# Performance work log

Measured on AMD Instinct MI355X. Metric: run time of the kernel, lower is better.

The kernel has to match this reference:

```python
import jax, jax.numpy as jnp
import numpy as np

B, LD = 256, 64
NO, LO = 10240, 32
NM, LM = 81920, 16
EO, EM = 81920, 327680
E, HID, H, Dh, V = 128, 256, 8, 16, 10000


def masked_mean(tokens, table):
    # tokens: [N, L] int; pad id = 0
    emb = table[tokens]                            # [N, L, E]
    mask = (tokens != 0)
    s = jnp.sum(emb * mask[..., None].astype(emb.dtype), axis=1)
    lens = jnp.maximum(jnp.sum(mask, axis=1), 1).astype(emb.dtype)
    return s / lens[:, None]


def segment_softmax(scores, seg, num_segments):
    # scores: [E, ...]; softmax over entries sharing seg id (PyG softmax)
    m = jax.ops.segment_max(scores, seg, num_segments=num_segments)
    e = jnp.exp(scores - m[seg])
    s = jax.ops.segment_sum(e, seg, num_segments=num_segments)
    return e / (s[seg] + 1e-16)


def gcn_conv(x, W, b, src, dst, n):
    # PyG GCNConv: normalize=True, add_self_loops=True
    xw = x @ W
    loops = jnp.arange(n, dtype=src.dtype)
    s2 = jnp.concatenate([src, loops])
    d2 = jnp.concatenate([dst, loops])
    deg = jax.ops.segment_sum(jnp.ones_like(d2, dtype=x.dtype), d2, num_segments=n)
    dinv = deg ** -0.5  # deg >= 1 due to self loops
    norm = dinv[s2] * dinv[d2]
    out = jax.ops.segment_sum(xw[s2] * norm[:, None], d2, num_segments=n)
    return out + b


def transformer_conv(x, Wq, bq, Wk, bk, Wv, bv, Wskip, bskip, src, dst, n):
    q = (x @ Wq + bq).reshape(n, H, Dh)
    k = (x @ Wk + bk).reshape(n, H, Dh)
    v = (x @ Wv + bv).reshape(n, H, Dh)
    score = jnp.sum(q[dst] * k[src], axis=-1) / jnp.sqrt(jnp.asarray(Dh, x.dtype))  # [E, H]
    alpha = segment_softmax(score, dst, n)
    agg = jax.ops.segment_sum(alpha[:, :, None] * v[src], dst, num_segments=n)  # [n, H, Dh]
    return agg.reshape(n, H * Dh) + x @ Wskip + bskip


def global_attention(x, Wg, bg, seg, num_segments):
    gate = x @ Wg + bg                              # [N, 1]
    a = segment_softmax(gate, seg, num_segments)
    return jax.ops.segment_sum(a * x, seg, num_segments=num_segments)


def setup_inputs():
    key = jax.random.key(0)
    ks = jax.random.split(key, 20)
    sc = lambda k, shape: jax.random.normal(k, shape, dtype=jnp.float32) * 0.05
    inp = {
        "desc_tokens": jax.random.randint(ks[0], (B, LD), 0, V, dtype=jnp.int32),
        "x_tokens": jax.random.randint(ks[1], (NO, LO), 0, V, dtype=jnp.int32),
        "mini_tokens": jax.random.randint(ks[2], (NM, LM), 0, V, dtype=jnp.int32),
        "src": jax.random.randint(ks[3], (EO,), 0, NO, dtype=jnp.int32),
        "dst": jax.random.randint(ks[4], (EO,), 0, NO, dtype=jnp.int32),
        "mini_src": jax.random.randint(ks[5], (EM,), 0, NM, dtype=jnp.int32),
        "mini_dst": jax.random.randint(ks[6], (EM,), 0, NM, dtype=jnp.int32),
        "mini_batch": (jnp.arange(NM, dtype=jnp.int32) // (NM // NO)),
        "node_batch": (jnp.arange(NO, dtype=jnp.int32) // (NO // B)),
        "desc_table": sc(ks[7], (V, E)),
        "code_table": sc(ks[8], (V, E)),
        "code_table2": sc(ks[9], (V, E)),
        "Wq": sc(ks[10], (E, H * Dh)), "bq": jnp.zeros((H * Dh,), jnp.float32),
        "Wk": sc(ks[11], (E, H * Dh)), "bk": jnp.zeros((H * Dh,), jnp.float32),
        "Wv": sc(ks[12], (E, H * Dh)), "bv": jnp.zeros((H * Dh,), jnp.float32),
        "Wskip": sc(ks[13], (E, H * Dh)), "bskip": jnp.zeros((H * Dh,), jnp.float32),
        "W2": sc(ks[14], (E, HID)), "b2": jnp.zeros((HID,), jnp.float32),
        "W3": sc(ks[15], (HID, E)), "b3": jnp.zeros((E,), jnp.float32),
        "Wg": sc(ks[16], (E, 1)), "bg": jnp.zeros((1,), jnp.float32),
    }
    return inp


def reference(desc_tokens, x_tokens, mini_tokens, src, dst, mini_src, mini_dst,
              mini_batch, node_batch, desc_table, code_table, code_table2,
              Wq, bq, Wk, bk, Wv, bv, Wskip, bskip, W2, b2, W3, b3, Wg, bg):
    # encode_desc: embedding + masked mean pool -> [B, E]
    h_n = masked_mean(desc_tokens, desc_table)
    # encode_code_graph
    stmt_emb = masked_mean(x_tokens, code_table2)          # [NO, E]
    mini_emb = masked_mean(mini_tokens, code_table)        # [NM, E]
    mini_hidden = transformer_conv(mini_emb, Wq, bq, Wk, bk, Wv, bv,
                                   Wskip, bskip, mini_src, mini_dst, NM)
    mini_fn = global_attention(mini_hidden, Wg, bg, mini_batch, NO)  # [NO, E]
    mini_fn = (mini_fn + stmt_emb) * 0.5
    h = jax.nn.relu(gcn_conv(mini_fn, W2, b2, src, dst, NO))
    final_stmt = gcn_conv(h, W3, b3, src, dst, NO)
    fn_repr = global_attention(final_stmt, Wg, bg, node_batch, B)    # [B, E]
    # cosine similarity (torch eps=1e-8 clamps each norm)
    na = jnp.maximum(jnp.linalg.norm(fn_repr, axis=-1), 1e-8)
    nb = jnp.maximum(jnp.linalg.norm(h_n, axis=-1), 1e-8)
    return jnp.sum(fn_repr * h_n, axis=-1) / (na * nb)
```

## Files before the change

### kernel.cpp

```cpp
#include <hip/hip_runtime.h>
#include <hip/hip_bf16.h>
#include <math.h>

#define BB   256
#define LDE  64
#define NO   10240
#define LO   32
#define NM   81920
#define LM   16
#define EO   81920
#define EM   327680
#define ED   128
#define HIDD 256
#define NH   8
#define DH   16
#define VV   10000

static inline int nblk(long long n, int b) { return (int)((n + b - 1) / b); }

typedef __attribute__((ext_vector_type(8))) short short8;
typedef __attribute__((ext_vector_type(4))) float f32x4;

static __device__ __forceinline__ unsigned short bf16_rne(float f) {
  unsigned u = __float_as_uint(f);
  return (unsigned short)((u + 0x7fffu + ((u >> 16) & 1u)) >> 16);
}
static __device__ __forceinline__ float bf16_to_f(unsigned short h) {
  return __uint_as_float(((unsigned)h) << 16);
}
static __device__ __forceinline__ float4 b4f(ushort4 h) {
  return make_float4(bf16_to_f(h.x), bf16_to_f(h.y), bf16_to_f(h.z), bf16_to_f(h.w));
}
static __device__ __forceinline__ ushort4 f4b(float4 v) {
  return make_ushort4(bf16_rne(v.x), bf16_rne(v.y), bf16_rne(v.z), bf16_rne(v.w));
}

static __device__ __forceinline__ void gl_lds16(const void* g, void* l) {
  __builtin_amdgcn_global_load_lds(
      (const __attribute__((address_space(1))) unsigned int*)g,
      (__attribute__((address_space(3))) unsigned int*)l, 16, 0, 0);
}

struct ConvArgs {
  const float *Wq, *Wk, *Wv, *Ws, *W2, *W3;
  const float *bq, *bk, *bv, *bs;
  short8* frag;
  float* bias512;
  const float* t1; unsigned short* o1;
  const float* t2; unsigned short* o2;
  int* hist;
};
#define TBLK (2 * VV * ED / 4 / 256)
#define ZBLK ((NM + NO) / 256)
__global__ void __launch_bounds__(256)
conv_all_k(ConvArgs A) {
  int b = blockIdx.x;
  if (b < 32) {
    int g = b * 256 + threadIdx.x;
    int lane = g & 63, f = g >> 6;
    int jl = f & 7, kb = (f >> 3) & 3, ch = f >> 5;
    int cf = ch * 8 + jl;
    int c = cf * 16 + (lane & 15);
    int k0 = kb * 32 + ((lane >> 4) << 3);
    const float* wp; int cm;
    if (c < 128)      { wp = A.Wq; cm = c; }
    else if (c < 384) { int u = c - 128, t = u & 7;
                        wp = (t < 4) ? A.Wk : A.Wv; cm = (u >> 3) * 4 + (t & 3); }
    else              { wp = A.Ws; cm = c - 384; }
    short8 h;
    #pragma unroll
    for (int j = 0; j < 8; ++j)
      h[j] = (short)bf16_rne(wp[(size_t)(k0 + j) * 128 + cm]);
    A.frag[g] = h;
  } else if (b < 64) {
    int g = (b - 32) * 256 + threadIdx.x;
    const float* wp; int M, dstbase, gg;
    if (g < 4096) { wp = A.W2; M = 256; dstbase = 8192;  gg = g; }
    else          { wp = A.W3; M = 128; dstbase = 12288; gg = g - 4096; }
    int lane = gg & 63, fid = gg >> 6;
    int nt = fid % (M / 16), kb = fid / (M / 16);
    int n = nt * 16 + (lane & 15);
    int k0 = kb * 32 + ((lane >> 4) << 3);
    short8 h;
    #pragma unroll
    for (int j = 0; j < 8; ++j)
      h[j] = (short)bf16_rne(wp[(size_t)(k0 + j) * M + n]);
    A.frag[dstbase + gg] = h;
  } else if (b < 64 + TBLK) {
    int q = (b - 64) * 256 + threadIdx.x;
    const int NT = VV * ED / 4;
    if (q < NT) {
      float4 v = *(const float4*)(A.t1 + (size_t)q * 4);
      *(ushort4*)(A.o1 + (size_t)q * 4) = f4b(v);
    } else if (q < 2 * NT) {
      int q2 = q - NT;
      float4 v = *(const float4*)(A.t2 + (size_t)q2 * 4);
      *(ushort4*)(A.o2 + (size_t)q2 * 4) = f4b(v);
    }
  } else if (b < 64 + TBLK + ZBLK) {
    int i = (b - 64 - TBLK) * 256 + threadIdx.x;
    if (i < NM + NO) A.hist[i] = 0;
  } else {
    for (int c = threadIdx.x; c < 512; c += 256) {
      float v;
      if (c < 128)      v = A.bq[c];
      else if (c < 384) { int u = c - 128, t = u & 7;
                          v = (t < 4) ? A.bk[(u >> 3) * 4 + t] : A.bv[(u >> 3) * 4 + (t & 3)]; }
      else              v = A.bs[c - 384];
      A.bias512[c] = v;
    }
  }
}

template<int L>
static __device__ __forceinline__ void embed_body_f(const int* __restrict__ tokens,
                                                    const float* __restrict__ table,
                                                    float* __restrict__ out, int blk) {
  const int r = threadIdx.x >> 5, lane = threadIdx.x & 31;
  const int n0 = blk * 8;
  __shared__ int toks[8][L];
  for (int i = threadIdx.x; i < 8 * L; i += 256)
    toks[i / L][i % L] = tokens[(size_t)n0 * L + i];
  __syncthreads();
  float4 acc = make_float4(0.f, 0.f, 0.f, 0.f);
  int cnt = 0;
  #pragma unroll
  for (int l = 0; l < L; ++l) {
    int t = toks[r][l];
    float4 v = *(const float4*)(table + (size_t)t * ED + lane * 4);
    float msk = (t != 0) ? 1.f : 0.f;
    cnt += (t != 0);
    acc.x = fmaf(msk, v.x, acc.x); acc.y = fmaf(msk, v.y, acc.y);
    acc.z = fmaf(msk, v.z, acc.z); acc.w = fmaf(msk, v.w, acc.w);
  }
  float inv = 1.f / (float)(cnt > 0 ? cnt : 1);
  acc.x *= inv; acc.y *= inv; acc.z *= inv; acc.w *= inv;
  *(float4*)(out + (size_t)(n0 + r) * ED + lane * 4) = acc;
}

template<int L>
static __device__ __forceinline__ void embed_body16(const int* __restrict__ tokens,
                                                    const unsigned short* __restrict__ table,
                                                    unsigned short* __restrict__ out, int blk) {
  const int r = threadIdx.x >> 4, lane = threadIdx.x & 15;
  const int n0 = blk * 16;
  __shared__ int toks[16][L];
  for (int i = threadIdx.x; i < 16 * L; i += 256)
    toks[i / L][i % L] = tokens[(size_t)n0 * L + i];
  __syncthreads();
  float acc[8] = {};
  int cnt = 0;
  #pragma unroll
  for (int l = 0; l < L; ++l) {
    int t = toks[r][l];
    short8 v = *(const short8*)(table + (size_t)t * ED + lane * 8);
    float msk = (t != 0) ? 1.f : 0.f;
    cnt += (t != 0);
    #pragma unroll
    for (int j = 0; j < 8; ++j)
      acc[j] = fmaf(msk, bf16_to_f((unsigned short)v[j]), acc[j]);
  }
  float inv = 1.f / (float)(cnt > 0 ? cnt : 1);
  short8 o;
  #pragma unroll
  for (int j = 0; j < 8; ++j) o[j] = (short)bf16_rne(acc[j] * inv);
  *(short8*)(out + (size_t)(n0 + r) * ED + lane * 8) = o;
}

#define HBLK ((EM + EO) / 256)
__global__ void __launch_bounds__(256)
embed_all_k(const int* __restrict__ desc_tokens, const float* __restrict__ desc_table,
            float* __restrict__ h_n,
            const int* __restrict__ x_tokens, const unsigned short* __restrict__ ctab2,
            unsigned short* __restrict__ stmt,
            const int* __restrict__ mini_tokens, const unsigned short* __restrict__ ctab,
            unsigned short* __restrict__ miniE,
            const int* __restrict__ mini_dst, const int* __restrict__ dst,
            int* __restrict__ histm, int* __restrict__ histo) {
  int b = blockIdx.x;
  if (b < HBLK) {
    int e = b * 256 + threadIdx.x;
    if (e < EM) atomicAdd(&histm[mini_dst[e]], 1);
    else        atomicAdd(&histo[dst[e - EM]], 1);
  }
  else if (b < HBLK + BB / 8) embed_body_f<LDE>(desc_tokens, desc_table, h_n, b - HBLK);
  else if (b < HBLK + BB / 8 + NO / 16)
    embed_body16<LO>(x_tokens, ctab2, stmt, b - HBLK - BB / 8);
  else embed_body16<LM>(mini_tokens, ctab, miniE, b - HBLK - BB / 8 - NO / 16);
}

__global__ void chunk_sum_k(const int* __restrict__ hist, int* __restrict__ partials, int N) {
  __shared__ int sd[256];
  int i = blockIdx.x * 256 + threadIdx.x;
  sd[threadIdx.x] = (i < N) ? hist[i] : 0;
  __syncthreads();
  for (int s = 128; s > 0; s >>= 1) {
    if (threadIdx.x < s) sd[threadIdx.x] += sd[threadIdx.x + s];
    __syncthreads();
  }
  if (threadIdx.x == 0) partials[blockIdx.x] = sd[0];
}
__global__ void scan_partials2_k(int* __restrict__ p) {
  __shared__ int sd[512];
  int base = (blockIdx.x == 0) ? 0 : NM / 256;
  int B    = (blockIdx.x == 0) ? NM / 256 : NO / 256;
  int t = threadIdx.x;
  int v = (t < B) ? p[base + t] : 0;
  sd[t] = v; __syncthreads();
  for (int off = 1; off < 512; off <<= 1) {
    int a = (t >= off) ? sd[t - off] : 0;
    __syncthreads();
    sd[t] += a;
    __syncthreads();
  }
  if (t < B) p[base + t] = sd[t] - v;
}
__global__ void scan_final2_k(const int* __restrict__ hist, const int* __restrict__ partials,
                              int* __restrict__ offsm, int* __restrict__ curm,
                              int* __restrict__ offso, int* __restrict__ curo,
                              float* __restrict__ dinv) {
  __shared__ int sd[256];
  int i = blockIdx.x * 256 + threadIdx.x;
  int v = hist[i];
  sd[threadIdx.x] = v; __syncthreads();
  for (int off = 1; off < 256; off <<= 1) {
    int a = (threadIdx.x >= off) ? sd[threadIdx.x - off] : 0;
    __syncthreads();
    sd[threadIdx.x] += a;
    __syncthreads();
  }
  int excl = sd[threadIdx.x] - v + partials[blockIdx.x];
  if (i < NM) {
    offsm[i] = excl; curm[i] = excl;
    if (i == NM - 1) offsm[NM] = excl + v;
  } else {
    int i2 = i - NM;
    offso[i2] = excl; curo[i2] = excl;
    if (i2 == NO - 1) offso[NO] = excl + v;
    dinv[i2] = 1.f / sqrtf(1.f + (float)v);
  }
}
__global__ void scatter2_k(const int* __restrict__ sm, const int* __restrict__ dm,
                           int* __restrict__ cm, int* __restrict__ km,
                           const int* __restrict__ so, const int* __restrict__ dd,
                           int* __restrict__ co, int* __restrict__ ko) {
  int e = blockIdx.x * 256 + threadIdx.x;
  if (e < EM) {
    int pos = atomicAdd(&cm[dm[e]], 1);
    km[pos] = sm[e];
  } else {
    int e2 = e - EM;
    if (e2 < EO) {
      int pos = atomicAdd(&co[dd[e2]], 1);
      ko[pos] = so[e2];
    }
  }
}

__global__ void __launch_bounds__(512)
qkvs_merged_k(const unsigned short* __restrict__ Ab, const short8* __restrict__ Wf,
              const float* __restrict__ bias512, unsigned short* __restrict__ out) {
  const int id = blockIdx.x;
  const int blk = (id & 7) * 80 + (id >> 3);
  const int n0 = blk * 128;
  const int tid = threadIdx.x;
  const int w = tid >> 6, lane = tid & 63;
  const int r = lane & 15, qd = lane >> 4;
  const int node = n0 + w * 16 + r;
  __shared__ short8 wlds[2048];
  char* myl = (char*)wlds + w * 4096;

  short8 a[4];
  #pragma unroll
  for (int kb = 0; kb < 4; ++kb)
    a[kb] = *(const short8*)(Ab + (size_t)node * ED + kb * 32 + qd * 8);

  for (int ch = 0; ch < 4; ++ch) {
    {
      const char* gs = (const char*)Wf + (size_t)ch * 32768
                     + (size_t)(w * 4) * 1024 + (size_t)lane * 16;
      char* ls = (char*)wlds + (w * 4) * 1024;
      #pragma unroll
      for (int t = 0; t < 4; ++t)
        gl_lds16(gs + t * 1024, ls + t * 1024);
    }
    __syncthreads();

    f32x4 acc[8];
    #pragma unroll
    for (int jl = 0; jl < 8; ++jl) acc[jl] = (f32x4){0.f, 0.f, 0.f, 0.f};
    #pragma unroll
    for (int kb = 0; kb < 4; ++kb)
      #pragma unroll
      for (int jl = 0; jl < 8; ++jl) {
        short8 wf = *(const short8*)((const char*)wlds
                      + ((size_t)((kb << 3) | jl) * 64 + lane) * 16);
        acc[jl] = __builtin_amdgcn_mfma_f32_16x16x32_bf16(wf, a[kb], acc[jl], 0, 0, 0);
      }
    __syncthreads();

    #pragma unroll
    for (int jl = 0; jl < 8; ++jl) {
      const int cf = ch * 8 + jl;
      const float4 bv = *(const float4*)(bias512 + cf * 16 + qd * 4);
      ushort4 o;
      o.x = bf16_rne(acc[jl][0] + bv.x);
      o.y = bf16_rne(acc[jl][1] + bv.y);
      o.z = bf16_rne(acc[jl][2] + bv.z);
      o.w = bf16_rne(acc[jl][3] + bv.w);
      *(ushort4*)(myl + r * 256 + ((jl * 32) ^ ((r & 7) << 5)) + qd * 8) = o;
    }
    #pragma unroll
    for (int t = 0; t < 4; ++t) {
      const int rr = t * 4 + qd;
      short8 v = *(const short8*)(myl + rr * 256 + (((lane & 15) * 16) ^ ((rr & 7) << 5)));
      *(short8*)(out + (size_t)(n0 + w * 16 + rr) * 512 + ch * 128 + (lane & 15) * 8) = v;
    }
    __syncthreads();
  }
}

template<bool RELU>
__global__ void __launch_bounds__(512)
mgemm_b_k(const unsigned short* __restrict__ Ab, const short8* __restrict__ Bh,
          const float* __restrict__ bias, unsigned short* __restrict__ C,
          int K, int M) {
  const int bn0 = blockIdx.x * 128;
  const int n0 = blockIdx.y * 128;
  const int tid = threadIdx.x;
  const int w = tid >> 6, lane = tid & 63;
  const int wm = (w & 3) * 2, wn = (w >> 2) * 4;
  const int r = lane & 15, qd = lane >> 4;
  const int NTm = M / 16;
  f32x4 acc[2][4];
  #pragma unroll
  for (int i = 0; i < 2; ++i)
    #pragma unroll
    for (int j = 0; j < 4; ++j) acc[i][j] = (f32x4){0.f, 0.f, 0.f, 0.f};
  const int kbn = K / 32;
  for (int kb = 0; kb < kbn; ++kb) {
    short8 bh[4];
    #pragma unroll
    for (int j = 0; j < 4; ++j)
      bh[j] = Bh[((size_t)kb * NTm + (bn0 >> 4) + wn + j) * 64 + lane];
    short8 a[2];
    #pragma unroll
    for (int i = 0; i < 2; ++i)
      a[i] = *(const short8*)(Ab + (size_t)(n0 + (wm + i) * 16 + r) * K + kb * 32 + qd * 8);
    #pragma unroll
    for (int i = 0; i < 2; ++i)
      #pragma unroll
      for (int j = 0; j < 4; ++j)
        acc[i][j] = __builtin_amdgcn_mfma_f32_16x16x32_bf16(bh[j], a[i], acc[i][j], 0, 0, 0);
  }
  #pragma unroll
  for (int i = 0; i < 2; ++i)
    #pragma unroll
    for (int j = 0; j < 4; ++j) {
      const int node = n0 + (wm + i) * 16 + r;
      const int colb = bn0 + (wn + j) * 16 + qd * 4;
      float4 bv = bias ? *(const float4*)(bias + colb) : make_float4(0.f, 0.f, 0.f, 0.f);
      float v0 = acc[i][j][0] + bv.x;
      float v1 = acc[i][j][1] + bv.y;
      float v2 = acc[i][j][2] + bv.z;
      float v3 = acc[i][j][3] + bv.w;
      if (RELU) {
        v0 = fmaxf(v0, 0.f); v1 = fmaxf(v1, 0.f);
        v2 = fmaxf(v2, 0.f); v3 = fmaxf(v3, 0.f);
      }
      ushort4 o = make_ushort4(bf16_rne(v0), bf16_rne(v1), bf16_rne(v2), bf16_rne(v3));
      *(ushort4*)(C + (size_t)node * M + colb) = o;
    }
}

__global__ void __launch_bounds__(128)
attn_fused_k(unsigned short* buf,
             const int* __restrict__ offs, const int* __restrict__ csr,
             const float* __restrict__ Wg, const float* __restrict__ bg,
             float* __restrict__ gateOut) {
  const int g = threadIdx.x >> 5, lane = threadIdx.x & 31;
  const int n = blockIdx.x * 4 + g;
  float4 q = b4f(*(const ushort4*)(buf + (size_t)n * 512 + lane * 4));
  float4 sk = b4f(*(const ushort4*)(buf + (size_t)n * 512 + 384 + lane * 4));
  float4 wg = *(const float4*)(Wg + lane * 4);
  int lo = offs[n], hi = offs[n + 1];
  float4 O = make_float4(0.f, 0.f, 0.f, 0.f);
  float m = -INFINITY, l = 0.f;
  for (int base = lo; base < hi; base += 4) {
    int rem = hi - base;
    int sidx[4];
    #pragma unroll
    for (int i = 0; i < 4; ++i) sidx[i] = (i < rem) ? csr[base + i] : 0;
    short8 kvr[4];
    #pragma unroll
    for (int i = 0; i < 4; ++i)
      kvr[i] = *(const short8*)(buf + (size_t)sidx[i] * 512 + 128 + lane * 8);
    float sc[4]; float4 vt[4];
    #pragma unroll
    for (int i = 0; i < 4; ++i) {
      float4 kt = make_float4(bf16_to_f((unsigned short)kvr[i][0]),
                              bf16_to_f((unsigned short)kvr[i][1]),
                              bf16_to_f((unsigned short)kvr[i][2]),
                              bf16_to_f((unsigned short)kvr[i][3]));
      vt[i] = make_float4(bf16_to_f((unsigned short)kvr[i][4]),
                          bf16_to_f((unsigned short)kvr[i][5]),
                          bf16_to_f((unsigned short)kvr[i][6]),
                          bf16_to_f((unsigned short)kvr[i][7]));
      float p = q.x * kt.x + q.y * kt.y + q.z * kt.z + q.w * kt.w;
      p += __shfl_xor(p, 1, 64);
      p += __shfl_xor(p, 2, 64);
      sc[i] = (i < rem) ? p * 0.25f : -INFINITY;
    }
    float mt = fmaxf(fmaxf(sc[0], sc[1]), fmaxf(sc[2], sc[3]));
    float mn = fmaxf(m, mt);
    float scale = __expf(m - mn);
    float pe[4];
    #pragma unroll
    for (int i = 0; i < 4; ++i) pe[i] = __expf(sc[i] - mn);
    l = l * scale + ((pe[0] + pe[1]) + (pe[2] + pe[3]));
    O.x = fmaf(pe[3], vt[3].x, fmaf(pe[2], vt[2].x, fmaf(pe[1], vt[1].x, fmaf(pe[0], vt[0].x, O.x * scale))));
    O.y = fmaf(pe[3], vt[3].y, fmaf(pe[2], vt[2].y, fmaf(pe[1], vt[1].y, fmaf(pe[0], vt[0].y, O.y * scale))));
    O.z = fmaf(pe[3], vt[3].z, fmaf(pe[2], vt[2].z, fmaf(pe[1], vt[1].z, fmaf(pe[0], vt[0].z, O.z * scale))));
    O.w = fmaf(pe[3], vt[3].w, fmaf(pe[2], vt[2].w, fmaf(pe[1], vt[1].w, fmaf(pe[0], vt[0].w, O.w * scale))));
    m = mn;
  }
  float inv = 1.f / (l + 1e-16f);
  float4 out = make_float4(O.x * inv + sk.x, O.y * inv + sk.y,
                           O.z * inv + sk.z, O.w * inv + sk.w);
  *(ushort4*)(buf + (size_t)n * 512 + lane * 4) = f4b(out);
  float ps = out.x * wg.x + out.y * wg.y + out.z * wg.z + out.w * wg.w;
  #pragma unroll
  for (int o = 1; o <= 16; o <<= 1) ps += __shfl_xor(ps, o, 64);
  if (lane == 0) gateOut[n] = ps + bg[0];
}

__global__ void __launch_bounds__(256)
gcn_gather_b_k(const unsigned short* __restrict__ x, const float* __restrict__ dinv,
               const int* __restrict__ offs, const int* __restrict__ csr,
               const float* __restrict__ bias, unsigned short* __restrict__ out,
               const float* __restrict__ Wg, const float* __restrict__ bg,
               float* __restrict__ gateOut) {
  const int wv = threadIdx.x >> 6, lane = threadIdx.x & 63;
  const int half = lane >> 5, cl = lane & 31;
  const int n = blockIdx.x * 4 + wv;
  float di = dinv[n];
  float4 acc = make_float4(0.f, 0.f, 0.f, 0.f);
  if (half == 0) {
    float4 xs = b4f(*(const ushort4*)(x + (size_t)n * ED + cl * 4));
    float w0 = di * di;
    acc = make_float4(w0 * xs.x, w0 * xs.y, w0 * xs.z, w0 * xs.w);
  }
  int lo = offs[n], hi = offs[n + 1];
  for (int base = lo; base < hi; base += 8) {
    int sidx[4]; bool ok[4];
    #pragma unroll
    for (int i = 0; i < 4; ++i) {
      int e = base + 2 * i + half;
      ok[i] = e < hi;
      sidx[i] = ok[i] ? csr[e] : 0;
    }
    float dw[4];
    #pragma unroll
    for (int i = 0; i < 4; ++i) dw[i] = ok[i] ? di * dinv[sidx[i]] : 0.f;
    ushort4 vr[4];
    #pragma unroll
    for (int i = 0; i < 4; ++i)
      vr[i] = *(const ushort4*)(x + (size_t)sidx[i] * ED + cl * 4);
    #pragma unroll
    for (int i = 0; i < 4; ++i) {
      float4 v = b4f(vr[i]);
      acc.x = fmaf(dw[i], v.x, acc.x); acc.y = fmaf(dw[i], v.y, acc.y);
      acc.z = fmaf(dw[i], v.z, acc.z); acc.w = fmaf(dw[i], v.w, acc.w);
    }
  }
  acc.x += __shfl_xor(acc.x, 32, 64); acc.y += __shfl_xor(acc.y, 32, 64);
  acc.z += __shfl_xor(acc.z, 32, 64); acc.w += __shfl_xor(acc.w, 32, 64);
  if (bias) {
    float4 b4 = *(const float4*)(bias + cl * 4);
    acc.x += b4.x; acc.y += b4.y; acc.z += b4.z; acc.w += b4.w;
  }
  if (half == 0)
    *(ushort4*)(out + (size_t)n * ED + cl * 4) = f4b(acc);
  if (gateOut) {
    float4 wg = *(const float4*)(Wg + cl * 4);
    float ps = acc.x * wg.x + acc.y * wg.y + acc.z * wg.z + acc.w * wg.w;
    #pragma unroll
    for (int o = 1; o <= 16; o <<= 1) ps += __shfl_xor(ps, o, 64);
    if (lane == 0) gateOut[n] = ps + bg[0];
  }
}

static __device__ __forceinline__ int lower_bound_d(const int* a, int n, int key) {
  int lo = 0, hi = n;
  while (lo < hi) { int mid = (lo + hi) >> 1; if (a[mid] < key) lo = mid + 1; else hi = mid; }
  return lo;
}
__global__ void __launch_bounds__(128)
gattn_comb_b_k(const unsigned short* __restrict__ xv, const float* __restrict__ gate,
               const int* __restrict__ seg, int Ntot,
               const unsigned short* __restrict__ other, unsigned short* __restrict__ out) {
  const int g = threadIdx.x >> 5, lane = threadIdx.x & 31;
  const int n = blockIdx.x * 4 + g;
  __shared__ int sh[4][2];
  if (lane == 0) {
    sh[g][0] = lower_bound_d(seg, Ntot, n);
    sh[g][1] = lower_bound_d(seg, Ntot, n + 1);
  }
  __syncthreads();
  int lo = sh[g][0], hi = sh[g][1];
  float m = -INFINITY;
  for (int j = lo; j < hi; ++j) m = fmaxf(m, gate[j]);
  float ssum = 0.f;
  for (int j = lo; j < hi; ++j) ssum += __expf(gate[j] - m);
  float inv = 1.f / (ssum + 1e-16f);
  float4 acc = make_float4(0.f, 0.f, 0.f, 0.f);
  for (int j = lo; j < hi; ++j) {
    float a = __expf(gate[j] - m) * inv;
    float4 v = b4f(*(const ushort4*)(xv + (size_t)j * 512 + lane * 4));
    acc.x = fmaf(a, v.x, acc.x); acc.y = fmaf(a, v.y, acc.y);
    acc.z = fmaf(a, v.z, acc.z); acc.w = fmaf(a, v.w, acc.w);
  }
  float4 o4 = b4f(*(const ushort4*)(other + (size_t)n * ED + lane * 4));
  acc.x = (acc.x + o4.x) * 0.5f; acc.y = (acc.y + o4.y) * 0.5f;
  acc.z = (acc.z + o4.z) * 0.5f; acc.w = (acc.w + o4.w) * 0.5f;
  *(ushort4*)(out + (size_t)n * ED + lane * 4) = f4b(acc);
}

__global__ void __launch_bounds__(128)
gattn_cos_k(const unsigned short* __restrict__ x, const float* __restrict__ gate,
            const int* __restrict__ seg, int Ntot,
            const float* __restrict__ hn, float* __restrict__ outp) {
  const int g = threadIdx.x >> 5, lane = threadIdx.x & 31;
  const int n = blockIdx.x * 4 + g;
  __shared__ int sh[4][2];
  if (lane == 0) {
    sh[g][0] = lower_bound_d(seg, Ntot, n);
    sh[g][1] = lower_bound_d(seg, Ntot, n + 1);
  }
  __syncthreads();
  int lo = sh[g][0], hi = sh[g][1];
  float m = -INFINITY;
  for (int j = lo; j < hi; ++j) m = fmaxf(m, gate[j]);
  float ssum = 0.f;
  for (int j = lo; j < hi; ++j) ssum += __expf(gate[j] - m);
  float inv = 1.f / (ssum + 1e-16f);
  float4 acc = make_float4(0.f, 0.f, 0.f, 0.f);
  for (int j = lo; j < hi; ++j) {
    float a = __expf(gate[j] - m) * inv;
    float4 v = b4f(*(const ushort4*)(x + (size_t)j * ED + lane * 4));
    acc.x = fmaf(a, v.x, acc.x); acc.y = fmaf(a, v.y, acc.y);
    acc.z = fmaf(a, v.z, acc.z); acc.w = fmaf(a, v.w, acc.w);
  }
  float4 hv = *(const float4*)(hn + (size_t)n * ED + lane * 4);
  float dot = acc.x * hv.x + acc.y * hv.y + acc.z * hv.z + acc.w * hv.w;
  float na  = acc.x * acc.x + acc.y * acc.y + acc.z * acc.z + acc.w * acc.w;
  float nb  = hv.x * hv.x + hv.y * hv.y + hv.z * hv.z + hv.w * hv.w;
  #pragma unroll
  for (int o = 1; o <= 16; o <<= 1) {
    dot += __shfl_xor(dot, o, 64);
    na  += __shfl_xor(na,  o, 64);
    nb  += __shfl_xor(nb,  o, 64);
  }
  if (lane == 0)
    outp[n] = dot / (fmaxf(sqrtf(na), 1e-8f) * fmaxf(sqrtf(nb), 1e-8f));
}

constexpr size_t OFF_HN    = 0;
constexpr size_t OFF_STMT  = OFF_HN    + (size_t)BB * ED;
constexpr size_t OFF_A     = OFF_STMT  + (size_t)NO * ED;
constexpr size_t OFF_CT    = OFF_A     + (size_t)NM * ED;
constexpr size_t OFF_QKVS  = OFF_CT    + (size_t)VV * ED;
constexpr size_t T0        = OFF_QKVS  + (size_t)NM * 256;
constexpr size_t OFF_GATE  = T0;
constexpr size_t OFF_GATE2 = OFF_GATE  + (size_t)NM;
constexpr size_t OFF_DINV  = OFF_GATE2 + (size_t)NO;
constexpr size_t OFF_HISTM = OFF_DINV  + (size_t)NO;
constexpr size_t OFF_HISTO = OFF_HISTM + (size_t)NM;
constexpr size_t OFF_OFFSM = OFF_HISTO + (size_t)NO;
constexpr size_t OFF_CURM  = OFF_OFFSM + (size_t)NM + 1;
constexpr size_t OFF_CSRM  = OFF_CURM  + (size_t)NM;
constexpr size_t OFF_OFFSO = OFF_CSRM  + (size_t)EM;
constexpr size_t OFF_CURO  = OFF_OFFSO + (size_t)NO + 1;
constexpr size_t OFF_CSRO  = OFF_CURO  + (size_t)NO;
constexpr size_t OFF_PART  = OFF_CSRO  + (size_t)EO;
constexpr size_t OFF_B512  = OFF_PART  + 512;
constexpr size_t OFF_WFHI  = OFF_B512  + 512;
constexpr size_t OFF_MFN   = OFF_A;
constexpr size_t OFF_AGG   = OFF_MFN   + (size_t)NO * ED;
constexpr size_t OFF_H     = OFF_AGG   + (size_t)NO * ED;
constexpr size_t OFF_T     = OFF_H     + (size_t)NO * HIDD;
constexpr size_t OFF_FIN   = OFF_T     + (size_t)NO * ED;

extern "C" void kernel_launch(void* const* d_in, const int* in_sizes, int n_in,
                              void* d_out, int out_size, void* d_ws, size_t ws_size,
                              hipStream_t stream) {
  const int* desc_tokens = (const int*)d_in[0];
  const int* x_tokens    = (const int*)d_in[1];
  const int* mini_tokens = (const int*)d_in[2];
  const int* src         = (const int*)d_in[3];
  const int* dst         = (const int*)d_in[4];
  const int* mini_src    = (const int*)d_in[5];
  const int* mini_dst    = (const int*)d_in[6];
  const int* mini_batch  = (const int*)d_in[7];
  const int* node_batch  = (const int*)d_in[8];
  const float* desc_table  = (const float*)d_in[9];
  const float* code_table  = (const float*)d_in[10];
  const float* code_table2 = (const float*)d_in[11];
  const float* Wq = (const float*)d_in[12]; const float* bq = (const float*)d_in[13];
  const float* Wk = (const float*)d_in[14]; const float* bk = (const float*)d_in[15];
  const float* Wv = (const float*)d_in[16]; const float* bv = (const float*)d_in[17];
  const float* Wskip = (const float*)d_in[18]; const float* bskip = (const float*)d_in[19];
  const float* W2 = (const float*)d_in[20]; const float* b2 = (const float*)d_in[21];
  const float* W3 = (const float*)d_in[22]; const float* b3 = (const float*)d_in[23];
  const float* Wg = (const float*)d_in[24]; const float* bg = (const float*)d_in[25];

  float* ws = (float*)d_ws;
  float* h_n   = ws + OFF_HN;
  unsigned short* stmt_b  = (unsigned short*)(ws + OFF_STMT);
  unsigned short* miniE_b = (unsigned short*)(ws + OFF_A);
  unsigned short* ctab_b  = (unsigned short*)(ws + OFF_CT);
  unsigned short* ctab2_b = ctab_b + (size_t)VV * ED;
  unsigned short* qkvs_b  = (unsigned short*)(ws + OFF_QKVS);
  float* gate  = ws + OFF_GATE;
  float* gate2 = ws + OFF_GATE2;
  float* dinv  = ws + OFF_DINV;
  int* histm = (int*)(ws + OFF_HISTM);
  int* histo = (int*)(ws + OFF_HISTO);
  int* offsm = (int*)(ws + OFF_OFFSM);
  int* curm  = (int*)(ws + OFF_CURM);
  int* csrm  = (int*)(ws + OFF_CSRM);
  int* offso = (int*)(ws + OFF_OFFSO);
  int* curo  = (int*)(ws + OFF_CURO);
  int* csro  = (int*)(ws + OFF_CSRO);
  int* part  = (int*)(ws + OFF_PART);
  float* bias512 = ws + OFF_B512;
  short8* wfrag = (short8*)(ws + OFF_WFHI);
  unsigned short* mini_fn_b = (unsigned short*)(ws + OFF_MFN);
  unsigned short* aggb_b    = (unsigned short*)(ws + OFF_AGG);
  unsigned short* hbuf_b    = (unsigned short*)(ws + OFF_H);
  unsigned short* tbuf_b    = (unsigned short*)(ws + OFF_T);
  unsigned short* finalS_b  = (unsigned short*)(ws + OFF_FIN);
  float* outp    = (float*)d_out;

  ConvArgs ca;
  ca.Wq = Wq; ca.Wk = Wk; ca.Wv = Wv; ca.Ws = Wskip; ca.W2 = W2; ca.W3 = W3;
  ca.bq = bq; ca.bk = bk; ca.bv = bv; ca.bs = bskip;
  ca.frag = wfrag; ca.bias512 = bias512;
  ca.t1 = code_table;  ca.o1 = ctab_b;
  ca.t2 = code_table2; ca.o2 = ctab2_b;
  ca.hist = histm;
  conv_all_k<<<64 + TBLK + ZBLK + 1, 256, 0, stream>>>(ca);

  embed_all_k<<<HBLK + BB / 8 + NO / 16 + NM / 16, 256, 0, stream>>>(
      desc_tokens, desc_table, h_n, x_tokens, ctab2_b, stmt_b,
      mini_tokens, ctab_b, miniE_b, mini_dst, dst, histm, histo);

  chunk_sum_k<<<(NM + NO) / 256, 256, 0, stream>>>(histm, part, NM + NO);
  scan_partials2_k<<<2, 512, 0, stream>>>(part);
  scan_final2_k<<<(NM + NO) / 256, 256, 0, stream>>>(histm, part, offsm, curm,
                                                     offso, curo, dinv);
  scatter2_k<<<nblk(EM + EO, 256), 256, 0, stream>>>(mini_src, mini_dst, curm, csrm,
                                                     src, dst, curo, csro);

  qkvs_merged_k<<<NM / 128, 512, 0, stream>>>(miniE_b, wfrag, bias512, qkvs_b);

  attn_fused_k<<<NM / 4, 128, 0, stream>>>(qkvs_b, offsm, csrm, Wg, bg, gate);

  gattn_comb_b_k<<<NO / 4, 128, 0, stream>>>(qkvs_b, gate, mini_batch, NM,
                                             stmt_b, mini_fn_b);

  gcn_gather_b_k<<<NO / 4, 256, 0, stream>>>(mini_fn_b, dinv, offso, csro, nullptr,
                                             aggb_b, nullptr, nullptr, nullptr);
  { dim3 g(HIDD / 128, NO / 128);
    mgemm_b_k<true><<<g, 512, 0, stream>>>(aggb_b, wfrag + 8192, b2, hbuf_b, ED, HIDD); }

  { dim3 g(1, NO / 128);
    mgemm_b_k<false><<<g, 512, 0, stream>>>(hbuf_b, wfrag + 12288, nullptr, tbuf_b, HIDD, ED); }
  gcn_gather_b_k<<<NO / 4, 256, 0, stream>>>(tbuf_b, dinv, offso, csro, b3, finalS_b,
                                             Wg, bg, gate2);

  gattn_cos_k<<<BB / 4, 128, 0, stream>>>(finalS_b, gate2, node_batch, NO, h_n, outp);
}
```

Baseline: 329.8 us.

## Merge chunk-sum into QKVS GEMM launch and batch embedding gathers

The histogram chunk-sum reduction is folded into the qkvs_merged_k launch as extra tail blocks, which removes one kernel launch and lets the scan's partial sums run alongside the GEMM. The embedding kernel now schedules the heavy embedding blocks before the histogram atomics. The bf16 embedding loop also issues 16 table loads before it accumulates them, giving more memory-level parallelism at the cost of extra registers. The GEMM kernel now has a branch in front and carries the 512-thread launch shape into the reduction blocks, where half the threads sit idle.

```diff
diff --git a/kernel.cpp b/kernel.cpp
--- a/kernel.cpp
+++ b/kernel.cpp
@@ -139,9 +139,9 @@
 }
 
 template<int L>
-static __device__ __forceinline__ void embed_body16(const int* __restrict__ tokens,
-                                                    const unsigned short* __restrict__ table,
-                                                    unsigned short* __restrict__ out, int blk) {
+static __device__ __forceinline__ void embed_body16b(const int* __restrict__ tokens,
+                                                     const unsigned short* __restrict__ table,
+                                                     unsigned short* __restrict__ out, int blk) {
   const int r = threadIdx.x >> 4, lane = threadIdx.x & 15;
   const int n0 = blk * 16;
   __shared__ int toks[16][L];
@@ -151,14 +151,22 @@
   float acc[8] = {};
   int cnt = 0;
   #pragma unroll
-  for (int l = 0; l < L; ++l) {
-    int t = toks[r][l];
-    short8 v = *(const short8*)(table + (size_t)t * ED + lane * 8);
-    float msk = (t != 0) ? 1.f : 0.f;
-    cnt += (t != 0);
-    #pragma unroll
-    for (int j = 0; j < 8; ++j)
-      acc[j] = fmaf(msk, bf16_to_f((unsigned short)v[j]), acc[j]);
+  for (int b0 = 0; b0 < L; b0 += 16) {
+    short8 vv[16];
+    #pragma unroll
+    for (int l = 0; l < 16; ++l) {
+      int t = toks[r][b0 + l];
+      vv[l] = *(const short8*)(table + (size_t)t * ED + lane * 8);
+    }
+    #pragma unroll
+    for (int l = 0; l < 16; ++l) {
+      int t = toks[r][b0 + l];
+      float msk = (t != 0) ? 1.f : 0.f;
+      cnt += (t != 0);
+      #pragma unroll
+      for (int j = 0; j < 8; ++j)
+        acc[j] = fmaf(msk, bf16_to_f((unsigned short)vv[l][j]), acc[j]);
+    }
   }
   float inv = 1.f / (float)(cnt > 0 ? cnt : 1);
   short8 o;
@@ -168,6 +176,8 @@
 }
 
 #define HBLK ((EM + EO) / 256)
+#define MBLK (NM / 16)
+#define XBLK (NO / 16)
 __global__ void __launch_bounds__(256)
 embed_all_k(const int* __restrict__ desc_tokens, const float* __restrict__ desc_table,
             float* __restrict__ h_n,
@@ -178,28 +188,17 @@
             const int* __restrict__ mini_dst, const int* __restrict__ dst,
             int* __restrict__ histm, int* __restrict__ histo) {
   int b = blockIdx.x;
-  if (b < HBLK) {
-    int e = b * 256 + threadIdx.x;
+  if (b < MBLK) embed_body16b<LM>(mini_tokens, ctab, miniE, b);
+  else if (b < MBLK + XBLK) embed_body16b<LO>(x_tokens, ctab2, stmt, b - MBLK);
+  else if (b < MBLK + XBLK + BB / 8)
+    embed_body_f<LDE>(desc_tokens, desc_table, h_n, b - MBLK - XBLK);
+  else {
+    int e = (b - MBLK - XBLK - BB / 8) * 256 + threadIdx.x;
     if (e < EM) atomicAdd(&histm[mini_dst[e]], 1);
     else        atomicAdd(&histo[dst[e - EM]], 1);
   }
-  else if (b < HBLK + BB / 8) embed_body_f<LDE>(desc_tokens, desc_table, h_n, b - HBLK);
-  else if (b < HBLK + BB / 8 + NO / 16)
-    embed_body16<LO>(x_tokens, ctab2, stmt, b - HBLK - BB / 8);
-  else embed_body16<LM>(mini_tokens, ctab, miniE, b - HBLK - BB / 8 - NO / 16);
-}
-
-__global__ void chunk_sum_k(const int* __restrict__ hist, int* __restrict__ partials, int N) {
-  __shared__ int sd[256];
-  int i = blockIdx.x * 256 + threadIdx.x;
-  sd[threadIdx.x] = (i < N) ? hist[i] : 0;
-  __syncthreads();
-  for (int s = 128; s > 0; s >>= 1) {
-    if (threadIdx.x < s) sd[threadIdx.x] += sd[threadIdx.x + s];
-    __syncthreads();
-  }
-  if (threadIdx.x == 0) partials[blockIdx.x] = sd[0];
-}
+}
+
 __global__ void scan_partials2_k(int* __restrict__ p) {
   __shared__ int sd[512];
   int base = (blockIdx.x == 0) ? 0 : NM / 256;
@@ -257,17 +256,33 @@
   }
 }
 
+#define QKVSB (NM / 128)
+#define CSUMB ((NM + NO) / 256)
 __global__ void __launch_bounds__(512)
 qkvs_merged_k(const unsigned short* __restrict__ Ab, const short8* __restrict__ Wf,
-              const float* __restrict__ bias512, unsigned short* __restrict__ out) {
+              const float* __restrict__ bias512, unsigned short* __restrict__ out,
+              const int* __restrict__ hist, int* __restrict__ part) {
+  __shared__ short8 wlds[2048];
+  const int tid = threadIdx.x;
+  if (blockIdx.x >= QKVSB) {
+    int* sd = (int*)wlds;
+    const int cb = blockIdx.x - QKVSB;
+    const int i = cb * 256 + (tid & 255);
+    if (tid < 256) sd[tid] = (i < NM + NO) ? hist[i] : 0;
+    __syncthreads();
+    for (int s = 128; s > 0; s >>= 1) {
+      if (tid < s) sd[tid] += sd[tid + s];
+      __syncthreads();
+    }
+    if (tid == 0) part[cb] = sd[0];
+    return;
+  }
   const int id = blockIdx.x;
   const int blk = (id & 7) * 80 + (id >> 3);
   const int n0 = blk * 128;
-  const int tid = threadIdx.x;
   const int w = tid >> 6, lane = tid & 63;
   const int r = lane & 15, qd = lane >> 4;
   const int node = n0 + w * 16 + r;
-  __shared__ short8 wlds[2048];
   char* myl = (char*)wlds + w * 4096;
 
   short8 a[4];
@@ -651,19 +666,19 @@
   ca.hist = histm;
   conv_all_k<<<64 + TBLK + ZBLK + 1, 256, 0, stream>>>(ca);
 
-  embed_all_k<<<HBLK + BB / 8 + NO / 16 + NM / 16, 256, 0, stream>>>(
+  embed_all_k<<<MBLK + XBLK + BB / 8 + HBLK, 256, 0, stream>>>(
       desc_tokens, desc_table, h_n, x_tokens, ctab2_b, stmt_b,
       mini_tokens, ctab_b, miniE_b, mini_dst, dst, histm, histo);
 
-  chunk_sum_k<<<(NM + NO) / 256, 256, 0, stream>>>(histm, part, NM + NO);
+  qkvs_merged_k<<<QKVSB + CSUMB, 512, 0, stream>>>(miniE_b, wfrag, bias512, qkvs_b,
+                                                   histm, part);
+
   scan_partials2_k<<<2, 512, 0, stream>>>(part);
   scan_final2_k<<<(NM + NO) / 256, 256, 0, stream>>>(histm, part, offsm, curm,
                                                      offso, curo, dinv);
   scatter2_k<<<nblk(EM + EO, 256), 256, 0, stream>>>(mini_src, mini_dst, curm, csrm,
                                                      src, dst, curo, csro);
 
-  qkvs_merged_k<<<NM / 128, 512, 0, stream>>>(miniE_b, wfrag, bias512, qkvs_b);
-
   attn_fused_k<<<NM / 4, 128, 0, stream>>>(qkvs_b, offsm, csrm, Wg, bg, gate);
 
   gattn_comb_b_k<<<NO / 4, 128, 0, stream>>>(qkvs_b, gate, mini_batch, NM,
```

After: 327.6 us. Within noise of the previous version (-0.7%).
